# Kernel tuning notes

Hardware: AMD Instinct MI355X
Metric: run time of the kernel (lower is better)

## Reference

```python
import jax, jax.numpy as jnp
import numpy as np
from jax import lax

K = 5  # kernel size
PAD = (K - 1) // 2


def setup_inputs() -> dict:
    key = jax.random.key(0)
    k1, k2, k3 = jax.random.split(key, 3)
    B, C, H, W = 16, 3, 256, 256
    x = jax.random.normal(k1, (B, C, H, W), dtype=jnp.float32)
    # Conv2d(3 -> 25, kernel=5) params, PyTorch-style fan-in init scale
    fan_in = C * K * K
    bound = 1.0 / np.sqrt(fan_in)
    conv_w = jax.random.uniform(k2, (K * K, C, K, K), dtype=jnp.float32, minval=-bound, maxval=bound)
    conv_b = jax.random.uniform(k3, (K * K,), dtype=jnp.float32, minval=-bound, maxval=bound)
    return {"x": x, "conv_w": conv_w, "conv_b": conv_b}


def reference(x, conv_w, conv_b):
    B, C, H, W = x.shape
    # weights = conv(x): [B, 25, H, W], one scalar weight per tap per pixel
    w = lax.conv_general_dilated(
        x, conv_w, window_strides=(1, 1), padding=((PAD, PAD), (PAD, PAD)),
        dimension_numbers=("NCHW", "OIHW", "NCHW"),
    ) + conv_b[None, :, None, None]
    # dynamic per-pixel 5x5 weighted neighborhood aggregation (zero-padded)
    xp = jnp.pad(x, ((0, 0), (0, 0), (PAD, PAD), (PAD, PAD)))
    out = jnp.zeros_like(x)
    k = 0
    for i in range(K):
        for j in range(K):
            # w[:, k] broadcasts over channels; xp slice is the (i,j)-shifted input
            out = out + w[:, k:k + 1] * xp[:, :, i:i + H, j:j + W]
            k += 1
    return out + x  # residual
```

## Files before the change

kernel.cpp:

```cpp
#include <hip/hip_runtime.h>
#include <stdint.h>

typedef __fp16    half2v __attribute__((ext_vector_type(2)));
typedef _Float16  f16x8  __attribute__((ext_vector_type(8)));
typedef float     f32x4  __attribute__((ext_vector_type(4)));
typedef uint32_t  u32x4  __attribute__((ext_vector_type(4)));

#define KSZ    5
#define NBATCH 16
#define NC     3
#define NH     256
#define NW     256
#define TW     16
#define TH     16
#define TROWS  20
#define TWRD   12
#define CPLANE (TROWS * TWRD)
#define COPYW  (NC * CPLANE)
#define PTS    20
#define NUNIT  (COPYW / 2)

__device__ __forceinline__ uint32_t pack_f16x2(float lo, float hi) {
    half2v h = __builtin_amdgcn_cvt_pkrtz(lo, hi);
    return __builtin_bit_cast(uint32_t, h);
}

__device__ __forceinline__ float fdot2(uint32_t w, uint32_t v, float acc) {
#if __has_builtin(__builtin_amdgcn_fdot2)
    return __builtin_amdgcn_fdot2(__builtin_bit_cast(half2v, w),
                                  __builtin_bit_cast(half2v, v), acc, false);
#else
    half2v a = __builtin_bit_cast(half2v, w);
    half2v b = __builtin_bit_cast(half2v, v);
    return acc + (float)a.x * (float)b.x + (float)a.y * (float)b.y;
#endif
}

__device__ __forceinline__ int pair_of(int s, int d) {
    return (d < 2) ? (2 * s + d) : (8 + 2 * s + (d - 2));
}

__global__ void prep_AB(const float* __restrict__ cw, const float* __restrict__ cb,
                        uint32_t* __restrict__ Atab, float* __restrict__ cbv)
{
    int idx = threadIdx.x + blockIdx.x * 256;
    if (idx < 1536) {
        int d  = idx & 3;
        int fl = (idx >> 2) & 15;
        int s  = (idx >> 6) & 3;
        int t3 = idx >> 8;
        int c  = t3 % 3, mt = t3 / 3;
        int vf = mt * 16 + fl;
        int P  = pair_of(s, d);
        float lo = 0.0f, hi = 0.0f;
        if (vf < 30 && (vf % 6) != 5 && P < 15) {
            int f = (vf / 6) * 5 + (vf % 6);
            int i = P / 3, q = P - 3 * i;
            const float* base = cw + f * 75 + c * 25 + i * 5;
            lo = base[2 * q];
            if (q < 2) hi = base[2 * q + 1];
        }
        Atab[idx] = pack_f16x2(lo, hi);
    } else if (idx < 1568) {
        int vf = idx - 1536;
        float v = 0.0f;
        if (vf < 30 && (vf % 6) != 5) v = cb[(vf / 6) * 5 + (vf % 6)];
        cbv[vf] = v;
    }
}

__global__ __launch_bounds__(256, 6)
void highorder22(const float* __restrict__ x,
                 const uint32_t* __restrict__ Atab,
                 const float* __restrict__ cbv,
                 float* __restrict__ out)
{
    __shared__ uint32_t lds_t[2 * COPYW];
    __shared__ uint32_t pbuf[TH * 16 * PTS];

    const int tid = threadIdx.x;
    const int l   = tid & 63;
    const int w   = tid >> 6;
    const int fl  = l & 15;
    const int s   = l >> 4;

    const int bx  = blockIdx.x & 15;
    const int by  = (blockIdx.x >> 4) & 15;
    const int b   = blockIdx.x >> 8;
    const int bw0 = bx * TW;
    const int bh0 = by * TH;

    const float* xb = x + (size_t)b * NC * NH * NW;

    u32x4 afr[6];
    const u32x4* At4 = (const u32x4*)Atab;
    #pragma unroll
    for (int t3 = 0; t3 < 6; ++t3)
        afr[t3] = At4[(t3 * 4 + s) * 16 + fl];
    const f32x4* cbv4 = (const f32x4*)cbv;
    const f32x4 cbA = cbv4[s];
    const f32x4 cbB = cbv4[4 + s];

    #pragma unroll
    for (int it = 0; it < 2; ++it) {
        int u = tid + it * 256;
        if (u < NUNIT) {
            int c   = u / 120;
            int rem = u - c * 120;
            int r   = rem / 6;
            int j   = rem - r * 6;
            int gh  = bh0 + r - 2;
            int g0  = bw0 + 4 * j - 2;
            bool rowok = (unsigned)gh < NH;
            const float* row = xb + c * NH * NW + gh * NW;
            float x0, x1, x2, x3, x4;
            if (rowok && g0 >= 0 && g0 + 4 < NW) {
                f32x4 v = *reinterpret_cast<const f32x4*>(row + g0);
                x0 = v[0]; x1 = v[1]; x2 = v[2]; x3 = v[3];
                x4 = row[g0 + 4];
            } else {
                x0 = (rowok && (unsigned)(g0)     < NW) ? row[g0]     : 0.0f;
                x1 = (rowok && (unsigned)(g0 + 1) < NW) ? row[g0 + 1] : 0.0f;
                x2 = (rowok && (unsigned)(g0 + 2) < NW) ? row[g0 + 2] : 0.0f;
                x3 = (rowok && (unsigned)(g0 + 3) < NW) ? row[g0 + 3] : 0.0f;
                x4 = (rowok && (unsigned)(g0 + 4) < NW) ? row[g0 + 4] : 0.0f;
            }
            const int idx0 = 2 * u;
            uint2 wa; wa.x = pack_f16x2(x0, x1); wa.y = pack_f16x2(x2, x3);
            uint2 wb; wb.x = pack_f16x2(x1, x2); wb.y = pack_f16x2(x3, x4);
            *reinterpret_cast<uint2*>(&lds_t[idx0])         = wa;
            *reinterpret_cast<uint2*>(&lds_t[COPYW + idx0]) = wb;
        }
    }
    __syncthreads();

    int woff[4];
    #pragma unroll
    for (int d = 0; d < 4; ++d) {
        int P = pair_of(s, d);
        int i = P / 3, q = P - 3 * i;
        woff[d] = (P == 15) ? 0 : (i * TWRD + q);
    }
    const int abase = ((fl & 1) ? COPYW : 0) + (fl >> 1);

    #pragma unroll
    for (int g = 0; g < 4; ++g) {
        const int py = w * 4 + g;
        const int bg = abase + py * TWRD;

        u32x4 bv[3];
        #pragma unroll
        for (int c = 0; c < 3; ++c)
            #pragma unroll
            for (int d = 0; d < 4; ++d)
                bv[c][d] = lds_t[bg + c * CPLANE + woff[d]];

        f32x4 a0 = cbA, a1 = cbB;
        #pragma unroll
        for (int c = 0; c < 3; ++c) {
            f16x8 B = __builtin_bit_cast(f16x8, bv[c]);
            a0 = __builtin_amdgcn_mfma_f32_16x16x32_f16(
                     __builtin_bit_cast(f16x8, afr[c]),     B, a0, 0, 0, 0);
            a1 = __builtin_amdgcn_mfma_f32_16x16x32_f16(
                     __builtin_bit_cast(f16x8, afr[3 + c]), B, a1, 0, 0, 0);
        }

        uint32_t wq0 = pack_f16x2(a0[0], a0[1]);
        uint32_t wq1 = pack_f16x2(a0[2], a0[3]);
        uint32_t wq2 = pack_f16x2(a1[0], a1[1]);
        uint32_t wq3 = pack_f16x2(a1[2], a1[3]);

        const int pb = (py * 16 + fl) * PTS;
        uint2 w01; w01.x = wq0; w01.y = wq1;
        uint2 w23; w23.x = wq2; w23.y = wq3;
        *reinterpret_cast<uint2*>(&pbuf[pb + 2 * s])     = w01;
        *reinterpret_cast<uint2*>(&pbuf[pb + 8 + 2 * s]) = w23;
    }

    const int px  = tid & 15;
    const int py2 = tid >> 4;
    const uint32_t* basep = lds_t + ((px & 1) ? COPYW : 0) + (px >> 1);

    uint32_t nb[45];
    #pragma unroll
    for (int c = 0; c < NC; ++c)
        #pragma unroll
        for (int i = 0; i < KSZ; ++i)
            #pragma unroll
            for (int q = 0; q < 3; ++q)
                nb[c * 15 + i * 3 + q] =
                    basep[c * CPLANE + (py2 + i) * TWRD + q];

    __syncthreads();

    u32x4 wp4[4];
    const int rb = (py2 * 16 + px) * PTS;
    #pragma unroll
    for (int r = 0; r < 4; ++r)
        wp4[r] = *reinterpret_cast<const u32x4*>(&pbuf[rb + 4 * r]);

    float* ob = out + (size_t)b * NC * NH * NW
                    + (size_t)(bh0 + py2) * NW + (bw0 + px);
    #pragma unroll
    for (int c = 0; c < NC; ++c) {
        half2v ctr = __builtin_bit_cast(half2v, nb[c * 15 + 7]);
        float sumA = (float)ctr.x;
        float sumB = 0.0f;
        #pragma unroll
        for (int t = 0; t < 8; ++t)
            sumA = fdot2(wp4[t >> 2][t & 3], nb[c * 15 + t], sumA);
        #pragma unroll
        for (int t = 8; t < 15; ++t)
            sumB = fdot2(wp4[t >> 2][t & 3], nb[c * 15 + t], sumB);
        ob[(size_t)c * NH * NW] = sumA + sumB;
    }
}

extern "C" void kernel_launch(void* const* d_in, const int* in_sizes, int n_in,
                              void* d_out, int out_size, void* d_ws, size_t ws_size,
                              hipStream_t stream)
{
    const float* x  = (const float*)d_in[0];
    const float* cw = (const float*)d_in[1];
    const float* cb = (const float*)d_in[2];
    float* out      = (float*)d_out;
    uint32_t* Atab  = (uint32_t*)d_ws;
    float*    cbv   = (float*)((char*)d_ws + 6144);

    prep_AB<<<7, 256, 0, stream>>>(cw, cb, Atab, cbv);

    dim3 grid(NBATCH * (NH / TH) * (NW / TW));
    highorder22<<<grid, 256, 0, stream>>>(x, Atab, cbv, out);
}
```

Before: 28.01 us.

## Give each wavefront a private halo tile to drop block-wide barriers

Each of the four wavefronts now loads its own 8-row halo strip into a private LDS region and uses its own slice of the weight buffer. The two __syncthreads are replaced by wave-local lgkmcnt waits plus scheduling barriers. This removes block-level synchronisation stalls but duplicates halo loads: 8 rows per 4 output rows instead of 20 per 16. It also increases LDS use and lowers the occupancy hint from 6 to 5.

```diff
diff --git a/kernel.cpp b/kernel.cpp
--- a/kernel.cpp
+++ b/kernel.cpp
@@ -13,12 +13,14 @@
 #define NW     256
 #define TW     16
 #define TH     16
-#define TROWS  20
-#define TWRD   12
-#define CPLANE (TROWS * TWRD)
-#define COPYW  (NC * CPLANE)
+#define SWRD   12
+#define SROWS  8
+#define SCPL   (SROWS * SWRD)
+#define SCOPY  (NC * SCPL)
+#define WREG   (2 * SCOPY)
 #define PTS    20
-#define NUNIT  (COPYW / 2)
+#define PPW    (64 * PTS)
+#define NUNITW 144
 
 __device__ __forceinline__ uint32_t pack_f16x2(float lo, float hi) {
     half2v h = __builtin_amdgcn_cvt_pkrtz(lo, hi);
@@ -69,18 +71,18 @@
     }
 }
 
-__global__ __launch_bounds__(256, 6)
-void highorder22(const float* __restrict__ x,
+__global__ __launch_bounds__(256, 5)
+void highorder23(const float* __restrict__ x,
                  const uint32_t* __restrict__ Atab,
                  const float* __restrict__ cbv,
                  float* __restrict__ out)
 {
-    __shared__ uint32_t lds_t[2 * COPYW];
-    __shared__ uint32_t pbuf[TH * 16 * PTS];
+    __shared__ uint32_t lds_t[4 * WREG];
+    __shared__ uint32_t pbuf[4 * PPW];
 
     const int tid = threadIdx.x;
     const int l   = tid & 63;
-    const int w   = tid >> 6;
+    const int wid = tid >> 6;
     const int fl  = l & 15;
     const int s   = l >> 4;
 
@@ -88,9 +90,11 @@
     const int by  = (blockIdx.x >> 4) & 15;
     const int b   = blockIdx.x >> 8;
     const int bw0 = bx * TW;
-    const int bh0 = by * TH;
+    const int bh0 = by * TH + wid * 4;
 
     const float* xb = x + (size_t)b * NC * NH * NW;
+    uint32_t* lw = lds_t + wid * WREG;
+    uint32_t* pw = pbuf + wid * PPW;
 
     u32x4 afr[6];
     const u32x4* At4 = (const u32x4*)Atab;
@@ -102,11 +106,11 @@
     const f32x4 cbB = cbv4[4 + s];
 
     #pragma unroll
-    for (int it = 0; it < 2; ++it) {
-        int u = tid + it * 256;
-        if (u < NUNIT) {
-            int c   = u / 120;
-            int rem = u - c * 120;
+    for (int it = 0; it < 3; ++it) {
+        int u = l + it * 64;
+        if (u < NUNITW) {
+            int c   = u / 48;
+            int rem = u - c * 48;
             int r   = rem / 6;
             int j   = rem - r * 6;
             int gh  = bh0 + r - 2;
@@ -125,35 +129,35 @@
                 x3 = (rowok && (unsigned)(g0 + 3) < NW) ? row[g0 + 3] : 0.0f;
                 x4 = (rowok && (unsigned)(g0 + 4) < NW) ? row[g0 + 4] : 0.0f;
             }
-            const int idx0 = 2 * u;
+            const int idx0 = c * SCPL + r * SWRD + 2 * j;
             uint2 wa; wa.x = pack_f16x2(x0, x1); wa.y = pack_f16x2(x2, x3);
             uint2 wb; wb.x = pack_f16x2(x1, x2); wb.y = pack_f16x2(x3, x4);
-            *reinterpret_cast<uint2*>(&lds_t[idx0])         = wa;
-            *reinterpret_cast<uint2*>(&lds_t[COPYW + idx0]) = wb;
+            *reinterpret_cast<uint2*>(&lw[idx0])         = wa;
+            *reinterpret_cast<uint2*>(&lw[SCOPY + idx0]) = wb;
         }
     }
-    __syncthreads();
+    asm volatile("s_waitcnt lgkmcnt(0)" ::: "memory");
+    __builtin_amdgcn_sched_barrier(0);
 
     int woff[4];
     #pragma unroll
     for (int d = 0; d < 4; ++d) {
         int P = pair_of(s, d);
         int i = P / 3, q = P - 3 * i;
-        woff[d] = (P == 15) ? 0 : (i * TWRD + q);
-    }
-    const int abase = ((fl & 1) ? COPYW : 0) + (fl >> 1);
+        woff[d] = (P == 15) ? 0 : (i * SWRD + q);
+    }
+    const int abase = ((fl & 1) ? SCOPY : 0) + (fl >> 1);
 
     #pragma unroll
     for (int g = 0; g < 4; ++g) {
-        const int py = w * 4 + g;
-        const int bg = abase + py * TWRD;
+        const int bg = abase + g * SWRD;
 
         u32x4 bv[3];
         #pragma unroll
         for (int c = 0; c < 3; ++c)
             #pragma unroll
             for (int d = 0; d < 4; ++d)
-                bv[c][d] = lds_t[bg + c * CPLANE + woff[d]];
+                bv[c][d] = lw[bg + c * SCPL + woff[d]];
 
         f32x4 a0 = cbA, a1 = cbB;
         #pragma unroll
@@ -170,16 +174,16 @@
         uint32_t wq2 = pack_f16x2(a1[0], a1[1]);
         uint32_t wq3 = pack_f16x2(a1[2], a1[3]);
 
-        const int pb = (py * 16 + fl) * PTS;
+        const int pb = (g * 16 + fl) * PTS;
         uint2 w01; w01.x = wq0; w01.y = wq1;
         uint2 w23; w23.x = wq2; w23.y = wq3;
-        *reinterpret_cast<uint2*>(&pbuf[pb + 2 * s])     = w01;
-        *reinterpret_cast<uint2*>(&pbuf[pb + 8 + 2 * s]) = w23;
-    }
-
-    const int px  = tid & 15;
-    const int py2 = tid >> 4;
-    const uint32_t* basep = lds_t + ((px & 1) ? COPYW : 0) + (px >> 1);
+        *reinterpret_cast<uint2*>(&pw[pb + 2 * s])     = w01;
+        *reinterpret_cast<uint2*>(&pw[pb + 8 + 2 * s]) = w23;
+    }
+
+    const int px  = l & 15;
+    const int py2 = l >> 4;
+    const uint32_t* basep = lw + ((px & 1) ? SCOPY : 0) + (px >> 1);
 
     uint32_t nb[45];
     #pragma unroll
@@ -189,15 +193,16 @@
             #pragma unroll
             for (int q = 0; q < 3; ++q)
                 nb[c * 15 + i * 3 + q] =
-                    basep[c * CPLANE + (py2 + i) * TWRD + q];
-
-    __syncthreads();
+                    basep[c * SCPL + (py2 + i) * SWRD + q];
+
+    asm volatile("s_waitcnt lgkmcnt(0)" ::: "memory");
+    __builtin_amdgcn_sched_barrier(0);
 
     u32x4 wp4[4];
     const int rb = (py2 * 16 + px) * PTS;
     #pragma unroll
     for (int r = 0; r < 4; ++r)
-        wp4[r] = *reinterpret_cast<const u32x4*>(&pbuf[rb + 4 * r]);
+        wp4[r] = *reinterpret_cast<const u32x4*>(&pw[rb + 4 * r]);
 
     float* ob = out + (size_t)b * NC * NH * NW
                     + (size_t)(bh0 + py2) * NW + (bw0 + px);
@@ -230,5 +235,5 @@
     prep_AB<<<7, 256, 0, stream>>>(cw, cb, Atab, cbv);
 
     dim3 grid(NBATCH * (NH / TH) * (NW / TW));
-    highorder22<<<grid, 256, 0, stream>>>(x, Atab, cbv, out);
-}
+    highorder23<<<grid, 256, 0, stream>>>(x, Atab, cbv, out);
+}
```

Result: slower. 31.09 us (+11.0%).
